# Kernel optimization log

Measured on AMD Instinct MI355X. Metric: run time of the kernel, lower is better.

## Reference

```python
import jax, jax.numpy as jnp
import numpy as np

B, N, K = 8, 2048, 16
C_IN, HID, C_OUT = 128, 128, 128
MSG_DIM = 2 * C_IN + 3


def setup_inputs() -> dict:
    key = jax.random.key(0)
    ks = jax.random.split(key, 9)
    h = jax.random.normal(ks[0], (B, N, C_IN), dtype=jnp.float32)
    pos = jax.random.normal(ks[1], (B, N, 3), dtype=jnp.float32)
    idx = jax.random.randint(ks[2], (B, N, K), 0, N, dtype=jnp.int64)
    # MLP params (Linear: y = x @ W.T + b; store as (in, out) for einsum-free matmul)
    s1 = 1.0 / np.sqrt(MSG_DIM)
    s2 = 1.0 / np.sqrt(HID)
    W1 = jax.random.uniform(ks[3], (MSG_DIM, HID), minval=-s1, maxval=s1, dtype=jnp.float32)
    b1 = jax.random.uniform(ks[4], (HID,), minval=-s1, maxval=s1, dtype=jnp.float32)
    W2 = jax.random.uniform(ks[5], (HID, C_OUT), minval=-s2, maxval=s2, dtype=jnp.float32)
    b2 = jax.random.uniform(ks[6], (C_OUT,), minval=-s2, maxval=s2, dtype=jnp.float32)
    gamma = jnp.ones((C_OUT,), dtype=jnp.float32)
    beta = jnp.zeros((C_OUT,), dtype=jnp.float32)
    return {"h": h, "pos": pos, "idx": idx, "W1": W1, "b1": b1,
            "W2": W2, "b2": b2, "gamma": gamma, "beta": beta}


def _gather(feats, idx):
    # feats: (B,N,C), idx: (B,N,k) -> (B,N,k,C)
    return jax.vmap(lambda f, i: f[i])(feats, idx)


def _layernorm(x, gamma, beta, eps=1e-5):
    mu = jnp.mean(x, axis=-1, keepdims=True)
    var = jnp.mean(jnp.square(x - mu), axis=-1, keepdims=True)
    return (x - mu) * jax.lax.rsqrt(var + eps) * gamma + beta


def reference(h, pos, idx, W1, b1, W2, b2, gamma, beta):
    # h: (B,N,C), pos: (B,N,3), idx: (B,N,k)
    h_j = _gather(h, idx)                      # (B,N,k,C)
    rel = _gather(pos, idx) - pos[:, :, None]  # (B,N,k,3)
    h_i = jnp.broadcast_to(h[:, :, None, :], h_j.shape)
    msg = jnp.concatenate([h_i, h_j - h_i, rel], axis=-1)   # (B,N,k,2C+3)
    x = jax.nn.gelu(msg @ W1 + b1, approximate=False)       # (B,N,k,H)
    x = jax.nn.gelu(x @ W2 + b2, approximate=False)         # (B,N,k,O)
    out = jnp.max(x, axis=2)                                 # (B,N,O)
    return _layernorm(out, gamma, beta)
```

## Files before the change

kernel.cpp:

```cpp
#include <hip/hip_runtime.h>

#define NPTS 2048
#define KNBR 16

typedef __attribute__((ext_vector_type(8))) short bf16x8;
typedef __attribute__((ext_vector_type(4))) float f32x4;
union U8 { bf16x8 v; unsigned u[4]; };

static __device__ __forceinline__ unsigned pk2(float lo, float hi) {
    unsigned r;
    asm("v_cvt_pk_bf16_f32 %0, %1, %2" : "=v"(r) : "v"(lo), "v"(hi));
    return r;
}

static __device__ __forceinline__ float gelu(float x) {
    float x2 = x * x;
    float u  = x * fmaf(x2, 0.044715f, 1.0f);
    float e  = __expf(u * -1.5957691216057308f);
    return x * __builtin_amdgcn_rcpf(1.0f + e);
}

#define STG 40
#define LDS_BYTES 147456

__global__ __launch_bounds__(1024, 4) void edgeconv_fused(
    const float* __restrict__ h, const float* __restrict__ pos,
    const int* __restrict__ idx,
    const float* __restrict__ W1, const float* __restrict__ W2,
    const float* __restrict__ b1, const float* __restrict__ b2,
    const float* __restrict__ gamma, const float* __restrict__ beta,
    float* __restrict__ out)
{
    extern __shared__ short lds[];
    float* ldsF = (float*)lds;
    const int tid = threadIdx.x, wave = tid >> 6, lane = tid & 63;
    const int quad = lane >> 4, lm = lane & 15;

    for (int c = tid; c < 6656; c += 1024) {
        const int l = c & 63, fi = c >> 6;
        const int lrow = (l >> 4) * 8, lcol = l & 15;
        U8 t;
        if (fi < 40) {
            int ks = fi % 5, nt = fi / 5;
            int row0 = 128 + ks * 32 + lrow, col = nt * 16 + lcol;
            #pragma unroll
            for (int p = 0; p < 4; ++p) {
                int r0 = row0 + 2 * p;
                float v0 = (r0     < 259) ? W1[r0 * 128 + col]       : 0.f;
                float v1 = (r0 + 1 < 259) ? W1[(r0 + 1) * 128 + col] : 0.f;
                t.u[p] = pk2(v0, v1);
            }
        } else if (fi < 72) {
            int f2 = fi - 40, ks = f2 & 3, nt = f2 >> 2;
            int row0 = ks * 32 + lrow, col = nt * 16 + lcol;
            #pragma unroll
            for (int p = 0; p < 4; ++p)
                t.u[p] = pk2(W2[(row0 + 2*p) * 128 + col],
                             W2[(row0 + 2*p + 1) * 128 + col]);
        } else {
            int f2 = fi - 72, ks = f2 & 3, nt = f2 >> 2;
            int row0 = ks * 32 + lrow, col = nt * 16 + lcol;
            #pragma unroll
            for (int p = 0; p < 4; ++p) {
                int r0 = row0 + 2 * p;
                float v0 = W1[r0 * 128 + col]       - W1[(r0 + 128) * 128 + col];
                float v1 = W1[(r0 + 1) * 128 + col] - W1[(r0 + 129) * 128 + col];
                t.u[p] = pk2(v0, v1);
            }
        }
        ((bf16x8*)lds)[c] = t.v;
    }

    float b1v[8], b2v[8];
    #pragma unroll
    for (int nt = 0; nt < 8; ++nt) {
        b1v[nt] = b1[nt * 16 + lm];
        b2v[nt] = b2[nt * 16 + lm];
    }
    const float gv0 = gamma[(quad * 2) * 16 + lm];
    const float gv1 = gamma[(quad * 2 + 1) * 16 + lm];
    const float be0 = beta[(quad * 2) * 16 + lm];
    const float be1 = beta[(quad * 2 + 1) * 16 + lm];

    __syncthreads();

    const bf16x8* w1frag  = (const bf16x8*)lds;
    const bf16x8* w2frag  = (const bf16x8*)lds + 2560;
    const bf16x8* w1dfrag = (const bf16x8*)lds + 4608;
    short* stg   = lds  + 36864 + wave * 1280;
    float* baseF = ldsF + 28672 + wave * 512;

    const int sb = (blockIdx.x & 7) * 32 + (blockIdx.x >> 3);
    const int node0 = sb * 64 + wave * 4;
    const int bidx = node0 >> 11;
    const float4* hb4 = (const float4*)h + (size_t)bidx * NPTS * 32;
    const float*  pb  = pos + (size_t)bidx * NPTS * 3;
    const int nloc = node0 & 2047;

    int idxv[4];
    #pragma unroll
    for (int ni = 0; ni < 4; ++ni)
        idxv[ni] = idx[(node0 + ni) * KNBR + lm];

    {
        const float4* hsrc = hb4 + (size_t)(nloc + (lm & 3)) * 32;
        bf16x8 af[4];
        #pragma unroll
        for (int ks = 0; ks < 4; ++ks) {
            float4 p0 = hsrc[ks * 8 + quad * 2];
            float4 p1 = hsrc[ks * 8 + quad * 2 + 1];
            U8 t;
            t.u[0] = pk2(p0.x, p0.y); t.u[1] = pk2(p0.z, p0.w);
            t.u[2] = pk2(p1.x, p1.y); t.u[3] = pk2(p1.z, p1.w);
            af[ks] = t.v;
        }
        f32x4 bacc[8];
        #pragma unroll
        for (int nt = 0; nt < 8; ++nt)
            bacc[nt] = (f32x4){b1v[nt], b1v[nt], b1v[nt], b1v[nt]};
        #pragma unroll
        for (int ks = 0; ks < 4; ++ks)
            #pragma unroll
            for (int nt = 0; nt < 8; ++nt)
                bacc[nt] = __builtin_amdgcn_mfma_f32_16x16x32_bf16(
                    af[ks], w1dfrag[(nt * 4 + ks) * 64 + lane], bacc[nt], 0, 0, 0);

        if (quad == 0)
            #pragma unroll
            for (int nt = 0; nt < 8; ++nt)
                #pragma unroll
                for (int r = 0; r < 4; ++r)
                    baseF[r * 128 + nt * 16 + lm] = bacc[nt][r];
    }
    __syncthreads();

    #pragma unroll
    for (int pr = 0; pr < 2; ++pr) {
        const int na = pr * 2, nb = pr * 2 + 1;
        const int ja = idxv[na], jb = idxv[nb];

        bf16x8 afA[4], afB[4];
        U8 rlA, rlB;
        {
            const float4* hjA4 = hb4 + (size_t)ja * 32;
            const float4* hjB4 = hb4 + (size_t)jb * 32;
            #pragma unroll
            for (int ks = 0; ks < 4; ++ks) {
                float4 j0 = hjA4[ks * 8 + quad * 2];
                float4 j1 = hjA4[ks * 8 + quad * 2 + 1];
                U8 t;
                t.u[0] = pk2(j0.x, j0.y); t.u[1] = pk2(j0.z, j0.w);
                t.u[2] = pk2(j1.x, j1.y); t.u[3] = pk2(j1.z, j1.w);
                afA[ks] = t.v;
                float4 k0 = hjB4[ks * 8 + quad * 2];
                float4 k1 = hjB4[ks * 8 + quad * 2 + 1];
                t.u[0] = pk2(k0.x, k0.y); t.u[1] = pk2(k0.z, k0.w);
                t.u[2] = pk2(k1.x, k1.y); t.u[3] = pk2(k1.z, k1.w);
                afB[ks] = t.v;
            }
            rlA.u[0] = 0; rlA.u[1] = 0; rlA.u[2] = 0; rlA.u[3] = 0;
            rlB.u[0] = 0; rlB.u[1] = 0; rlB.u[2] = 0; rlB.u[3] = 0;
            if (quad == 0) {
                int ia = nloc + na, ib = nloc + nb;
                rlA.u[0] = pk2(pb[3*ja]   - pb[3*ia],   pb[3*ja+1] - pb[3*ia+1]);
                rlA.u[1] = pk2(pb[3*ja+2] - pb[3*ia+2], 0.f);
                rlB.u[0] = pk2(pb[3*jb]   - pb[3*ib],   pb[3*jb+1] - pb[3*ib+1]);
                rlB.u[1] = pk2(pb[3*jb+2] - pb[3*ib+2], 0.f);
            }
        }

        bf16x8 a2A[4], a2B[4];
        #pragma unroll
        for (int ks2 = 0; ks2 < 4; ++ks2) {
            #pragma unroll
            for (int ntl = 0; ntl < 2; ++ntl) {
                const int nt = ks2 * 2 + ntl;
                float bA = baseF[na * 128 + nt * 16 + lm];
                float bB = baseF[nb * 128 + nt * 16 + lm];
                f32x4 cA = (f32x4){bA, bA, bA, bA};
                f32x4 cB = (f32x4){bB, bB, bB, bB};
                #pragma unroll
                for (int ks = 0; ks < 4; ++ks) {
                    bf16x8 w = w1frag[(nt * 5 + ks) * 64 + lane];
                    cA = __builtin_amdgcn_mfma_f32_16x16x32_bf16(afA[ks], w, cA, 0, 0, 0);
                    cB = __builtin_amdgcn_mfma_f32_16x16x32_bf16(afB[ks], w, cB, 0, 0, 0);
                }
                {
                    bf16x8 w = w1frag[(nt * 5 + 4) * 64 + lane];
                    cA = __builtin_amdgcn_mfma_f32_16x16x32_bf16(rlA.v, w, cA, 0, 0, 0);
                    cB = __builtin_amdgcn_mfma_f32_16x16x32_bf16(rlB.v, w, cB, 0, 0, 0);
                }
                #pragma unroll
                for (int r = 0; r < 4; ++r) {
                    float gA = gelu(cA[r]), gB = gelu(cB[r]);
                    stg[      (quad * 4 + r) * STG + ntl * 16 + lm] = (short)pk2(gA, gA);
                    stg[640 + (quad * 4 + r) * STG + ntl * 16 + lm] = (short)pk2(gB, gB);
                }
            }
            asm volatile("s_waitcnt lgkmcnt(0)" ::: "memory");
            a2A[ks2] = *(const bf16x8*)(stg +       lm * STG + quad * 8);
            a2B[ks2] = *(const bf16x8*)(stg + 640 + lm * STG + quad * 8);
            asm volatile("s_waitcnt lgkmcnt(0)" ::: "memory");
        }

        float vA[8], vB[8];
        #pragma unroll
        for (int nt = 0; nt < 8; ++nt) {
            f32x4 cA = (f32x4){0.f, 0.f, 0.f, 0.f};
            f32x4 cB = (f32x4){0.f, 0.f, 0.f, 0.f};
            #pragma unroll
            for (int ks = 0; ks < 4; ++ks) {
                bf16x8 w = w2frag[(nt * 4 + ks) * 64 + lane];
                cA = __builtin_amdgcn_mfma_f32_16x16x32_bf16(a2A[ks], w, cA, 0, 0, 0);
                cB = __builtin_amdgcn_mfma_f32_16x16x32_bf16(a2B[ks], w, cB, 0, 0, 0);
            }
            float mxA = fmaxf(fmaxf(cA[0], cA[1]), fmaxf(cA[2], cA[3]));
            float mnA = fminf(fminf(cA[0], cA[1]), fminf(cA[2], cA[3]));
            float mxB = fmaxf(fmaxf(cB[0], cB[1]), fmaxf(cB[2], cB[3]));
            float mnB = fminf(fminf(cB[0], cB[1]), fminf(cB[2], cB[3]));
            mxA = fmaxf(mxA, __shfl_xor(mxA, 16, 64));
            mxA = fmaxf(mxA, __shfl_xor(mxA, 32, 64));
            mnA = fminf(mnA, __shfl_xor(mnA, 16, 64));
            mnA = fminf(mnA, __shfl_xor(mnA, 32, 64));
            mxB = fmaxf(mxB, __shfl_xor(mxB, 16, 64));
            mxB = fmaxf(mxB, __shfl_xor(mxB, 32, 64));
            mnB = fminf(mnB, __shfl_xor(mnB, 16, 64));
            mnB = fminf(mnB, __shfl_xor(mnB, 32, 64));
            vA[nt] = fmaxf(gelu(mxA + b2v[nt]), gelu(mnA + b2v[nt]));
            vB[nt] = fmaxf(gelu(mxB + b2v[nt]), gelu(mnB + b2v[nt]));
        }

        #pragma unroll
        for (int u = 0; u < 2; ++u) {
            const float* v = u ? vB : vA;
            float s = 0.f, s2 = 0.f;
            #pragma unroll
            for (int nt = 0; nt < 8; ++nt) { s += v[nt]; s2 += v[nt] * v[nt]; }
            #pragma unroll
            for (int off = 1; off <= 8; off <<= 1) {
                s  += __shfl_xor(s,  off, 64);
                s2 += __shfl_xor(s2, off, 64);
            }
            const float mu  = s * (1.0f / 128.0f);
            const float var = s2 * (1.0f / 128.0f) - mu * mu;
            const float inv = rsqrtf(var + 1e-5f);
            float* orow = out + (size_t)(node0 + pr * 2 + u) * 128;
            orow[(quad * 2) * 16 + lm]     = (v[quad * 2]     - mu) * inv * gv0 + be0;
            orow[(quad * 2 + 1) * 16 + lm] = (v[quad * 2 + 1] - mu) * inv * gv1 + be1;
        }
    }
}

extern "C" void kernel_launch(void* const* d_in, const int* in_sizes, int n_in,
                              void* d_out, int out_size, void* d_ws, size_t ws_size,
                              hipStream_t stream) {
    const float* h     = (const float*)d_in[0];
    const float* pos   = (const float*)d_in[1];
    const int*   idx   = (const int*)  d_in[2];
    const float* W1    = (const float*)d_in[3];
    const float* b1    = (const float*)d_in[4];
    const float* W2    = (const float*)d_in[5];
    const float* b2    = (const float*)d_in[6];
    const float* gamma = (const float*)d_in[7];
    const float* beta  = (const float*)d_in[8];
    float* out = (float*)d_out;

    hipFuncSetAttribute((const void*)edgeconv_fused,
                        hipFuncAttributeMaxDynamicSharedMemorySize, LDS_BYTES);
    edgeconv_fused<<<256, 1024, LDS_BYTES, stream>>>(
        h, pos, idx, W1, W2, b1, b2, gamma, beta, out);
}
```

Baseline: 119.9 us.

## Transpose layer-1 MFMA and pass activations via lane shuffles instead of LDS staging

Swaps the operand order of the first-layer MFMAs so each lane holds four consecutive hidden channels of one edge. The GELU outputs can then be packed two per register and rearranged into the second-layer A-operand layout with cross-lane shuffles, replacing the per-wave LDS staging buffer and its waitcnt round-trips. The base and bias vectors are loaded and stored as float4 to match the transposed layout, and the staging area is dropped from the LDS allocation. This adds shuffle and select instructions, and the packed conversion removes the redundant duplicate-packing.

```diff
diff --git a/kernel.cpp b/kernel.cpp
--- a/kernel.cpp
+++ b/kernel.cpp
@@ -6,6 +6,7 @@
 typedef __attribute__((ext_vector_type(8))) short bf16x8;
 typedef __attribute__((ext_vector_type(4))) float f32x4;
 union U8 { bf16x8 v; unsigned u[4]; };
+union F4 { f32x4 v; float4 q; };
 
 static __device__ __forceinline__ unsigned pk2(float lo, float hi) {
     unsigned r;
@@ -20,8 +21,7 @@
     return x * __builtin_amdgcn_rcpf(1.0f + e);
 }
 
-#define STG 40
-#define LDS_BYTES 147456
+#define LDS_BYTES 139264
 
 __global__ __launch_bounds__(1024, 4) void edgeconv_fused(
     const float* __restrict__ h, const float* __restrict__ pos,
@@ -71,12 +71,9 @@
         ((bf16x8*)lds)[c] = t.v;
     }
 
-    float b1v[8], b2v[8];
+    float b2v[8];
     #pragma unroll
-    for (int nt = 0; nt < 8; ++nt) {
-        b1v[nt] = b1[nt * 16 + lm];
-        b2v[nt] = b2[nt * 16 + lm];
-    }
+    for (int nt = 0; nt < 8; ++nt) b2v[nt] = b2[nt * 16 + lm];
     const float gv0 = gamma[(quad * 2) * 16 + lm];
     const float gv1 = gamma[(quad * 2 + 1) * 16 + lm];
     const float be0 = beta[(quad * 2) * 16 + lm];
@@ -87,8 +84,7 @@
     const bf16x8* w1frag  = (const bf16x8*)lds;
     const bf16x8* w2frag  = (const bf16x8*)lds + 2560;
     const bf16x8* w1dfrag = (const bf16x8*)lds + 4608;
-    short* stg   = lds  + 36864 + wave * 1280;
-    float* baseF = ldsF + 28672 + wave * 512;
+    float* baseF = ldsF + 26624 + wave * 512;
 
     const int sb = (blockIdx.x & 7) * 32 + (blockIdx.x >> 3);
     const int node0 = sb * 64 + wave * 4;
@@ -101,6 +97,11 @@
     #pragma unroll
     for (int ni = 0; ni < 4; ++ni)
         idxv[ni] = idx[(node0 + ni) * KNBR + lm];
+
+    const int p   = quad & 1;
+    const int qhi = quad >> 1;
+    const int srcA = (p * 2 + (1 ^ qhi)) * 16 + lm;
+    const int srcB = (p * 2 + qhi) * 16 + lm;
 
     {
         const float4* hsrc = hb4 + (size_t)(nloc + (lm & 3)) * 32;
@@ -116,21 +117,23 @@
         }
         f32x4 bacc[8];
         #pragma unroll
-        for (int nt = 0; nt < 8; ++nt)
-            bacc[nt] = (f32x4){b1v[nt], b1v[nt], b1v[nt], b1v[nt]};
+        for (int nt = 0; nt < 8; ++nt) {
+            F4 bi; bi.q = *(const float4*)(b1 + nt * 16 + quad * 4);
+            bacc[nt] = bi.v;
+        }
         #pragma unroll
         for (int ks = 0; ks < 4; ++ks)
             #pragma unroll
             for (int nt = 0; nt < 8; ++nt)
                 bacc[nt] = __builtin_amdgcn_mfma_f32_16x16x32_bf16(
-                    af[ks], w1dfrag[(nt * 4 + ks) * 64 + lane], bacc[nt], 0, 0, 0);
-
-        if (quad == 0)
-            #pragma unroll
-            for (int nt = 0; nt < 8; ++nt)
-                #pragma unroll
-                for (int r = 0; r < 4; ++r)
-                    baseF[r * 128 + nt * 16 + lm] = bacc[nt][r];
+                    w1dfrag[(nt * 4 + ks) * 64 + lane], af[ks], bacc[nt], 0, 0, 0);
+
+        if (lm < 4)
+            #pragma unroll
+            for (int nt = 0; nt < 8; ++nt) {
+                F4 o; o.v = bacc[nt];
+                *(float4*)(baseF + lm * 128 + nt * 16 + quad * 4) = o.q;
+            }
     }
     __syncthreads();
 
@@ -171,36 +174,55 @@
 
         bf16x8 a2A[4], a2B[4];
         #pragma unroll
-        for (int ks2 = 0; ks2 < 4; ++ks2) {
-            #pragma unroll
-            for (int ntl = 0; ntl < 2; ++ntl) {
-                const int nt = ks2 * 2 + ntl;
-                float bA = baseF[na * 128 + nt * 16 + lm];
-                float bB = baseF[nb * 128 + nt * 16 + lm];
-                f32x4 cA = (f32x4){bA, bA, bA, bA};
-                f32x4 cB = (f32x4){bB, bB, bB, bB};
+        for (int k2 = 0; k2 < 4; ++k2) {
+            unsigned PA[2][2], PB[2][2];
+            #pragma unroll
+            for (int lnt = 0; lnt < 2; ++lnt) {
+                const int nt = k2 * 2 + lnt;
+                F4 iA, iB;
+                iA.q = *(const float4*)(baseF + na * 128 + nt * 16 + quad * 4);
+                iB.q = *(const float4*)(baseF + nb * 128 + nt * 16 + quad * 4);
+                f32x4 xA = iA.v, xB = iB.v;
                 #pragma unroll
                 for (int ks = 0; ks < 4; ++ks) {
                     bf16x8 w = w1frag[(nt * 5 + ks) * 64 + lane];
-                    cA = __builtin_amdgcn_mfma_f32_16x16x32_bf16(afA[ks], w, cA, 0, 0, 0);
-                    cB = __builtin_amdgcn_mfma_f32_16x16x32_bf16(afB[ks], w, cB, 0, 0, 0);
+                    xA = __builtin_amdgcn_mfma_f32_16x16x32_bf16(w, afA[ks], xA, 0, 0, 0);
+                    xB = __builtin_amdgcn_mfma_f32_16x16x32_bf16(w, afB[ks], xB, 0, 0, 0);
                 }
                 {
                     bf16x8 w = w1frag[(nt * 5 + 4) * 64 + lane];
-                    cA = __builtin_amdgcn_mfma_f32_16x16x32_bf16(rlA.v, w, cA, 0, 0, 0);
-                    cB = __builtin_amdgcn_mfma_f32_16x16x32_bf16(rlB.v, w, cB, 0, 0, 0);
+                    xA = __builtin_amdgcn_mfma_f32_16x16x32_bf16(w, rlA.v, xA, 0, 0, 0);
+                    xB = __builtin_amdgcn_mfma_f32_16x16x32_bf16(w, rlB.v, xB, 0, 0, 0);
                 }
-                #pragma unroll
-                for (int r = 0; r < 4; ++r) {
-                    float gA = gelu(cA[r]), gB = gelu(cB[r]);
-                    stg[      (quad * 4 + r) * STG + ntl * 16 + lm] = (short)pk2(gA, gA);
-                    stg[640 + (quad * 4 + r) * STG + ntl * 16 + lm] = (short)pk2(gB, gB);
-                }
-            }
-            asm volatile("s_waitcnt lgkmcnt(0)" ::: "memory");
-            a2A[ks2] = *(const bf16x8*)(stg +       lm * STG + quad * 8);
-            a2B[ks2] = *(const bf16x8*)(stg + 640 + lm * STG + quad * 8);
-            asm volatile("s_waitcnt lgkmcnt(0)" ::: "memory");
+                PA[lnt][0] = pk2(gelu(xA[0]), gelu(xA[1]));
+                PA[lnt][1] = pk2(gelu(xA[2]), gelu(xA[3]));
+                PB[lnt][0] = pk2(gelu(xB[0]), gelu(xB[1]));
+                PB[lnt][1] = pk2(gelu(xB[2]), gelu(xB[3]));
+            }
+            {
+                unsigned rA_ = (unsigned)__shfl((int)(p ? PA[0][0] : PA[1][0]), srcA, 64);
+                unsigned rB_ = (unsigned)__shfl((int)(p ? PA[1][0] : PA[0][0]), srcB, 64);
+                unsigned rC_ = (unsigned)__shfl((int)(p ? PA[0][1] : PA[1][1]), srcA, 64);
+                unsigned rD_ = (unsigned)__shfl((int)(p ? PA[1][1] : PA[0][1]), srcB, 64);
+                U8 ua;
+                ua.u[0] = qhi ? rA_ : rB_;
+                ua.u[1] = qhi ? rC_ : rD_;
+                ua.u[2] = qhi ? rB_ : rA_;
+                ua.u[3] = qhi ? rD_ : rC_;
+                a2A[k2] = ua.v;
+            }
+            {
+                unsigned rA_ = (unsigned)__shfl((int)(p ? PB[0][0] : PB[1][0]), srcA, 64);
+                unsigned rB_ = (unsigned)__shfl((int)(p ? PB[1][0] : PB[0][0]), srcB, 64);
+                unsigned rC_ = (unsigned)__shfl((int)(p ? PB[0][1] : PB[1][1]), srcA, 64);
+                unsigned rD_ = (unsigned)__shfl((int)(p ? PB[1][1] : PB[0][1]), srcB, 64);
+                U8 ub;
+                ub.u[0] = qhi ? rA_ : rB_;
+                ub.u[1] = qhi ? rC_ : rD_;
+                ub.u[2] = qhi ? rB_ : rA_;
+                ub.u[3] = qhi ? rD_ : rC_;
+                a2B[k2] = ub.v;
+            }
         }
 
         float vA[8], vB[8];
```

Result: slower. 123.4 us (+2.9%).
